# Optimization experiments

Hardware: AMD Instinct MI355X
Metric: run time of the kernel (lower is better)

The kernel has to match this reference:

```python
import jax, jax.numpy as jnp
import numpy as np

B, S, E = 2, 2048, 1024
H = 16
D = E // H  # head_dim = 64


def setup_inputs() -> dict:
    key = jax.random.key(0)
    ks = jax.random.split(key, 11)
    s = 1.0 / np.sqrt(E)
    return {
        "x": jax.random.normal(ks[0], (B, S, E), dtype=jnp.float32),
        "Wq": jax.random.uniform(ks[1], (E, E), jnp.float32, -s, s),
        "bq": jnp.zeros((E,), jnp.float32),
        "Wk": jax.random.uniform(ks[2], (E, E), jnp.float32, -s, s),
        "bk": jnp.zeros((E,), jnp.float32),
        "Wv": jax.random.uniform(ks[3], (E, E), jnp.float32, -s, s),
        "bv": jnp.zeros((E,), jnp.float32),
        "Wo": jax.random.uniform(ks[4], (E, E), jnp.float32, -s, s),
        "bo": jnp.zeros((E,), jnp.float32),
        "J_attn": jax.random.normal(ks[5], (H, D, D), jnp.float32) * 0.02,
        "lambda_attn": jnp.float32(0.5),
    }


def reference(x, Wq, bq, Wk, bk, Wv, bv, Wo, bo, J_attn, lambda_attn):
    b, s, _ = x.shape
    scale = jnp.sqrt(jnp.float32(D))

    def split_heads(y):  # [b,s,E] -> [b,H,s,D]
        return y.reshape(b, s, H, D).transpose(0, 2, 1, 3)

    Q = split_heads(x @ Wq.T + bq)
    K = split_heads(x @ Wk.T + bk)
    V = split_heads(x @ Wv.T + bv)

    attn_scores = jnp.einsum('bhid,bhjd->bhij', Q, K) / scale

    Qn = jnp.tanh(Q)
    Kn = jnp.tanh(K)
    # fold J into Qn first (small [H,D,D] contraction), then one big matmul
    QJ = jnp.einsum('bhid,hde->bhie', Qn, J_attn)
    delta = jnp.einsum('bhie,bhje->bhij', QJ, Kn)

    attn_scores = attn_scores + lambda_attn * delta
    attn_probs = jax.nn.softmax(attn_scores, axis=-1)

    out = jnp.einsum('bhij,bhjd->bhid', attn_probs, V)
    out = out.transpose(0, 2, 1, 3).reshape(b, s, E)
    return out @ Wo.T + bo
```

## Files before the change

kernel.cpp:

```cpp
#include <hip/hip_runtime.h>
#include <math.h>

#define NH 16

typedef __bf16 bf16x8 __attribute__((ext_vector_type(8)));
typedef float f32x4 __attribute__((ext_vector_type(4)));

__device__ __forceinline__ unsigned short f2bf(float f) {
  unsigned u = __float_as_uint(f);
  u += 0x7fffu + ((u >> 16) & 1u);
  return (unsigned short)(u >> 16);
}
__device__ __forceinline__ float bf2f(unsigned short h) {
  return __uint_as_float(((unsigned)h) << 16);
}
__device__ __forceinline__ float fast_tanh16(float x) {
  return 1.f - 2.f / (__expf(16.f * x) + 1.f);
}
__device__ __forceinline__ void gl_lds16(const void* g, void* l) {
  __builtin_amdgcn_global_load_lds((const __attribute__((address_space(1))) void*)g,
                                   (__attribute__((address_space(3))) void*)l, 16, 0, 0);
}
union Frag8 { bf16x8 v; unsigned short u[8]; };
union FragU { bf16x8 v; unsigned u[4]; };
union FragQ { bf16x8 v; unsigned long long q[2]; };

__global__ __launch_bounds__(256) void prep_all(const float* __restrict__ x,
                                                const float* __restrict__ Wq,
                                                const float* __restrict__ Wk,
                                                const float* __restrict__ Wv,
                                                const float* __restrict__ Wo,
                                                unsigned short* __restrict__ xh,
                                                unsigned short* __restrict__ wcat3,
                                                unsigned short* __restrict__ wocat)
{
  const int bid = blockIdx.x, tid = threadIdx.x;
  if (bid < 4096) {
    int i = bid * 256 + tid;
    float4 v = *(const float4*)&x[(size_t)i*4];
    ushort4 o;
    o.x = f2bf(v.x); o.y = f2bf(v.y); o.z = f2bf(v.z); o.w = f2bf(v.w);
    *(ushort4*)&xh[(size_t)i*4] = o;
  } else if (bid < 7168) {
    int i = (bid - 4096) * 256 + tid;
    int sel = i >> 18, loc = i & 262143;
    const float* src = (sel == 0) ? Wq : (sel == 1) ? Wk : Wv;
    float4 v = *(const float4*)&src[(size_t)loc*4];
    ushort4 o;
    o.x = f2bf(v.x); o.y = f2bf(v.y); o.z = f2bf(v.z); o.w = f2bf(v.w);
    *(ushort4*)&wcat3[(size_t)i*4] = o;
  } else {
    int i = (bid - 7168) * 256 + tid;
    int r = i >> 8, c = i & 255;
    float4 v = *(const float4*)&Wo[(size_t)r*1024 + c*4];
    ushort4 hi, lo;
    hi.x = f2bf(v.x); lo.x = f2bf(v.x - bf2f(hi.x));
    hi.y = f2bf(v.y); lo.y = f2bf(v.y - bf2f(hi.y));
    hi.z = f2bf(v.z); lo.z = f2bf(v.z - bf2f(hi.z));
    hi.w = f2bf(v.w); lo.w = f2bf(v.w - bf2f(hi.w));
    *(ushort4*)&wocat[(size_t)r*2048 + c*4]        = hi;
    *(ushort4*)&wocat[(size_t)r*2048 + 1024 + c*4] = lo;
  }
}

__global__ __launch_bounds__(256) void prep_jt(const float* __restrict__ J,
                                               const float* __restrict__ lam_p,
                                               unsigned short* __restrict__ Jt)
{
  __shared__ float T[64][65];
  const int h = blockIdx.x, tid = threadIdx.x;
  const float lam = lam_p[0];
#pragma unroll
  for (int c = 0; c < 4; ++c) {
    int i = tid + c*256;
    int d = i >> 4, e4 = i & 15;
    float4 v = *(const float4*)&J[(size_t)h*4096 + d*64 + e4*4];
    T[d][e4*4+0] = v.x; T[d][e4*4+1] = v.y; T[d][e4*4+2] = v.z; T[d][e4*4+3] = v.w;
  }
  __syncthreads();
  const int e = tid >> 2, d0 = (tid & 3) * 16;
#pragma unroll
  for (int j4 = 0; j4 < 4; ++j4) {
    ushort4 o;
    o.x = f2bf(lam * T[d0+j4*4+0][e]);
    o.y = f2bf(lam * T[d0+j4*4+1][e]);
    o.z = f2bf(lam * T[d0+j4*4+2][e]);
    o.w = f2bf(lam * T[d0+j4*4+3][e]);
    *(ushort4*)&Jt[((size_t)h*64 + e)*64 + d0 + j4*4] = o;
  }
}

__global__ __launch_bounds__(256) void gemm_qkv(const unsigned short* __restrict__ A,
                                                const unsigned short* __restrict__ W,
                                                const float* __restrict__ bq,
                                                const float* __restrict__ bk,
                                                const float* __restrict__ bv,
                                                unsigned short* __restrict__ Qcat,
                                                unsigned short* __restrict__ Kcat,
                                                unsigned short* __restrict__ Vt)
{
  __shared__ unsigned short S[16384];
  const int tid = threadIdx.x, lane = tid & 63, wq = tid >> 6;
  const int l15 = lane & 15, lq = lane >> 4;
  const int n0 = blockIdx.x * 128, m0 = blockIdx.y * 128;
  const int wr = (wq & 1) * 64, wc = (wq >> 1) * 64;
  const int mode = n0 >> 10;

  f32x4 acc[4][4];
#pragma unroll
  for (int mb = 0; mb < 4; ++mb)
#pragma unroll
    for (int nb = 0; nb < 4; ++nb) { f32x4 z = {0.f,0.f,0.f,0.f}; acc[mb][nb] = z; }

  const unsigned short* mat = (wq < 2) ? A : W;
  const int rbase = (wq < 2) ? m0 : n0;
  unsigned short* lbase = S + (wq >> 1) * 8192;
  const int srow = lane >> 3, sslot = lane & 7;

  for (int k0 = 0; k0 < 1024; k0 += 64) {
    __syncthreads();
#pragma unroll
    for (int t = 0; t < 8; ++t) {
      int row = (wq & 1) * 64 + t*8 + srow;
      int chunk = sslot ^ (row & 7);
      gl_lds16(mat + (size_t)(rbase + row)*1024 + k0 + chunk*8,
               lbase + ((wq & 1) * 64 + t*8) * 64);
    }
    __syncthreads();
#pragma unroll
    for (int kk = 0; kk < 2; ++kk) {
      int c = kk*4 + lq;
      bf16x8 af[4], bf_[4];
#pragma unroll
      for (int mb = 0; mb < 4; ++mb) {
        int m = wr + mb*16 + l15;
        af[mb] = *(const bf16x8*)&S[m*64 + (c ^ (m & 7))*8];
      }
#pragma unroll
      for (int nb = 0; nb < 4; ++nb) {
        int n = wc + nb*16 + l15;
        bf_[nb] = *(const bf16x8*)&S[8192 + n*64 + (c ^ (n & 7))*8];
      }
#pragma unroll
      for (int mb = 0; mb < 4; ++mb)
#pragma unroll
        for (int nb = 0; nb < 4; ++nb)
          acc[mb][nb] = __builtin_amdgcn_mfma_f32_16x16x32_bf16(af[mb], bf_[nb], acc[mb][nb], 0,0,0);
    }
  }

  const float* bias = (mode == 0) ? bq : (mode == 1) ? bk : bv;
  float bvv[4];
#pragma unroll
  for (int nb = 0; nb < 4; ++nb) bvv[nb] = bias[((n0 & 1023) + wc + nb*16 + l15)];

  if (mode == 2) {
#pragma unroll
    for (int mb = 0; mb < 4; ++mb) {
      int mrow = m0 + wr + mb*16 + lq*4;
      int b = mrow >> 11, s0 = mrow & 2047;
#pragma unroll
      for (int nb = 0; nb < 4; ++nb) {
        int n = (n0 & 1023) + wc + nb*16 + l15;
        int h = n >> 6, d = n & 63;
        ushort4 o;
        o.x = f2bf(acc[mb][nb][0] + bvv[nb]);
        o.y = f2bf(acc[mb][nb][1] + bvv[nb]);
        o.z = f2bf(acc[mb][nb][2] + bvv[nb]);
        o.w = f2bf(acc[mb][nb][3] + bvv[nb]);
        *(ushort4*)&Vt[((size_t)(b*NH + h)*64 + d)*2048 + s0] = o;
      }
    }
    return;
  }

#pragma unroll
  for (int mb = 0; mb < 4; ++mb) {
#pragma unroll
    for (int r = 0; r < 4; ++r) {
      int m = m0 + wr + mb*16 + lq*4 + r;
      int b = m >> 11, s = m & 2047;
#pragma unroll
      for (int nb = 0; nb < 4; ++nb) {
        float v = acc[mb][nb][r] + bvv[nb];
        int n = (n0 & 1023) + wc + nb*16 + l15;
        int h = n >> 6, d = n & 63;
        size_t row = ((size_t)(b*NH + h)*2048 + s)*128;
        if (mode == 0) {
          Qcat[row + d] = f2bf(v * 0.125f);
        } else {
          Kcat[row + d]      = f2bf(v);
          Kcat[row + 64 + d] = f2bf(1.f - 2.f / (__expf(2.f*v) + 1.f));
        }
      }
    }
  }
}

__global__ __launch_bounds__(256) void build_qj2(unsigned short* __restrict__ Qcat,
                                                 const unsigned short* __restrict__ Jt)
{
  const int tid = threadIdx.x, lane = tid & 63, wq = tid >> 6;
  const int l15 = lane & 15, lq = lane >> 4;
  const int bh = blockIdx.y, row0 = blockIdx.x * 128;
  const int h = bh & (NH-1);

  bf16x8 jf[4][2];
#pragma unroll
  for (int nb = 0; nb < 4; ++nb)
#pragma unroll
    for (int kst = 0; kst < 2; ++kst)
      jf[nb][kst] = *(const bf16x8*)&Jt[((size_t)h*64 + nb*16 + l15)*64 + kst*32 + lq*8];

  Frag8 af[2][2];
#pragma unroll
  for (int mb = 0; mb < 2; ++mb) {
    const unsigned short* qp = Qcat + ((size_t)(bh*2048 + row0 + wq*32 + mb*16 + l15))*128 + lq*8;
#pragma unroll
    for (int kst = 0; kst < 2; ++kst) {
      Frag8 raw;
      raw.v = *(const bf16x8*)(qp + kst*32);
#pragma unroll
      for (int j = 0; j < 8; ++j) {
        float t = fast_tanh16(bf2f(raw.u[j]));
        af[mb][kst].u[j] = (unsigned short)(__float_as_uint(t) >> 16);
      }
    }
  }

  f32x4 acc[2][4];
#pragma unroll
  for (int mb = 0; mb < 2; ++mb)
#pragma unroll
    for (int nb = 0; nb < 4; ++nb) { f32x4 z = {0.f,0.f,0.f,0.f}; acc[mb][nb] = z; }
#pragma unroll
  for (int kst = 0; kst < 2; ++kst)
#pragma unroll
    for (int mb = 0; mb < 2; ++mb)
#pragma unroll
      for (int nb = 0; nb < 4; ++nb)
        acc[mb][nb] = __builtin_amdgcn_mfma_f32_16x16x32_bf16(af[mb][kst].v, jf[nb][kst], acc[mb][nb], 0,0,0);

#pragma unroll
  for (int mb = 0; mb < 2; ++mb)
#pragma unroll
    for (int r = 0; r < 4; ++r) {
      size_t rowb = ((size_t)(bh*2048 + row0 + wq*32 + mb*16 + lq*4 + r))*128 + 64;
#pragma unroll
      for (int nb = 0; nb < 4; ++nb)
        Qcat[rowb + nb*16 + l15] = f2bf(acc[mb][nb][r]);
    }
}

__global__ __launch_bounds__(256, 4) void flash7(
    const unsigned short* __restrict__ Qcat, const unsigned short* __restrict__ Kcat,
    const unsigned short* __restrict__ Vt, float* __restrict__ OP0,
    float* __restrict__ OP1, float* __restrict__ OP2, float* __restrict__ lpart)
{
  __shared__ unsigned short Ks[64*128];
  __shared__ unsigned short Vs[64*64];
  const int tid = threadIdx.x, lane = tid & 63, wq = tid >> 6;
  const int l15 = lane & 15, lq = lane >> 4;
  const int bid = blockIdx.x;
  const int bh = (((bid >> 3) & 3) << 3) | (bid & 7);
  const int inner = bid >> 5;
  const int row0 = (inner & 15) * 128;
  const int ks = inner >> 4;
  const int jt0 = ks * 11;
  const int jtN = jt0 + ((ks < 2) ? 11 : 10);

  Frag8 qf[2][4];
#pragma unroll
  for (int nb = 0; nb < 2; ++nb) {
    const unsigned short* qp = Qcat + ((size_t)(bh*2048 + row0 + wq*32 + nb*16 + l15))*128 + lq*8;
#pragma unroll
    for (int kst = 0; kst < 4; ++kst)
      qf[nb][kst].v = *(const bf16x8*)(qp + kst*32);
  }

  f32x4 o[4][2];
  float lp[2] = {0.f, 0.f};
#pragma unroll
  for (int db = 0; db < 4; ++db)
#pragma unroll
    for (int nb = 0; nb < 2; ++nb) { f32x4 z = {0.f,0.f,0.f,0.f}; o[db][nb] = z; }

  const unsigned short* kgb = Kcat + ((size_t)bh*2048)*128;
  const unsigned short* vg  = Vt + (size_t)bh*64*2048;

  for (int jt = jt0; jt < jtN; ++jt) {
    __syncthreads();
#pragma unroll
    for (int t = 0; t < 4; ++t) {
      int g = (wq*4 + t)*4 + (lane >> 4);
      int slot = lane & 15;
      int chunk = (slot & 8) | ((slot ^ g) & 7);
      gl_lds16(kgb + (size_t)(jt*64 + g)*128 + chunk*8, Ks + (wq*4 + t)*512);
    }
#pragma unroll
    for (int t = 0; t < 2; ++t) {
      int rv = (wq*2 + t)*8 + (lane >> 3);
      int chunk = (lane & 7) ^ (rv & 7);
      gl_lds16(vg + (size_t)rv*2048 + jt*64 + chunk*8, Vs + (wq*2 + t)*512);
    }
    __syncthreads();

#pragma unroll
    for (int t = 0; t < 2; ++t) {
      unsigned P2[2][2][2];
#pragma unroll
      for (int kk = 0; kk < 2; ++kk) {
        const int kb = 2*t + kk;
        bf16x8 af[4];
#pragma unroll
        for (int kst = 0; kst < 4; ++kst) {
          int key = kb*16 + l15;
          int c = kst*4 + lq;
          int slot = (c & 8) | ((c ^ key) & 7);
          af[kst] = *(const bf16x8*)&Ks[key*128 + slot*8];
        }
        f32x4 s[2];
        { f32x4 z = {0.f,0.f,0.f,0.f}; s[0] = z; s[1] = z; }
#pragma unroll
        for (int kst = 0; kst < 4; ++kst) {
          s[0] = __builtin_amdgcn_mfma_f32_16x16x32_bf16(af[kst], qf[0][kst].v, s[0], 0,0,0);
          s[1] = __builtin_amdgcn_mfma_f32_16x16x32_bf16(af[kst], qf[1][kst].v, s[1], 0,0,0);
        }
#pragma unroll
        for (int nb = 0; nb < 2; ++nb) {
          float e0 = __expf(s[nb][0]), e1 = __expf(s[nb][1]);
          float e2 = __expf(s[nb][2]), e3 = __expf(s[nb][3]);
          unsigned pk0 = __builtin_amdgcn_perm(__float_as_uint(e1), __float_as_uint(e0), 0x07060302u);
          unsigned pk1 = __builtin_amdgcn_perm(__float_as_uint(e3), __float_as_uint(e2), 0x07060302u);
          lp[nb] += __uint_as_float(pk0 << 16) + __uint_as_float(pk0 & 0xffff0000u)
                  + __uint_as_float(pk1 << 16) + __uint_as_float(pk1 & 0xffff0000u);
          P2[nb][kk][0] = pk0;
          P2[nb][kk][1] = pk1;
        }
      }

      FragU bfr[2];
#pragma unroll
      for (int nb = 0; nb < 2; ++nb) {
        bfr[nb].u[0] = P2[nb][0][0];
        bfr[nb].u[1] = P2[nb][0][1];
        bfr[nb].u[2] = P2[nb][1][0];
        bfr[nb].u[3] = P2[nb][1][1];
      }
      const int c0 = 4*t + (lq >> 1);
      const int woff = 4*(lq & 1);
#pragma unroll
      for (int db = 0; db < 4; ++db) {
        int d = db*16 + l15;
        FragQ va;
        va.q[0] = *(const unsigned long long*)&Vs[d*64 + ((c0     ^ (d & 7))*8) + woff];
        va.q[1] = *(const unsigned long long*)&Vs[d*64 + (((c0+2) ^ (d & 7))*8) + woff];
        o[db][0] = __builtin_amdgcn_mfma_f32_16x16x32_bf16(va.v, bfr[0].v, o[db][0], 0,0,0);
        o[db][1] = __builtin_amdgcn_mfma_f32_16x16x32_bf16(va.v, bfr[1].v, o[db][1], 0,0,0);
      }
    }
  }

  float* OP = (ks == 0) ? OP0 : (ks == 1) ? OP1 : OP2;
#pragma unroll
  for (int nb = 0; nb < 2; ++nb) {
    float rs = lp[nb];
    rs += __shfl_xor(rs, 16, 64);
    rs += __shfl_xor(rs, 32, 64);
    int qrow = row0 + wq*32 + nb*16 + l15;
    if (lq == 0) lpart[(size_t)ks*65536 + bh*2048 + qrow] = rs;
#pragma unroll
    for (int db = 0; db < 4; ++db)
#pragma unroll
      for (int r = 0; r < 4; ++r) {
        int d = db*16 + lq*4 + r;
        OP[(size_t)(bh*64 + d)*2048 + qrow] = o[db][nb][r];
      }
  }
}

__global__ __launch_bounds__(256) void combine3(const float* __restrict__ OP0,
                                                const float* __restrict__ OP1,
                                                const float* __restrict__ OP2,
                                                const float* __restrict__ lpart,
                                                unsigned short* __restrict__ attcat)
{
  __shared__ float Ts[64*68];
  __shared__ float Ls[64];
  const int tid = threadIdx.x;
  const int bh = blockIdx.y, s0 = blockIdx.x * 64;
  const int b = bh >> 4, h = bh & (NH-1);
#pragma unroll
  for (int c = 0; c < 4; ++c) {
    int fid = tid + c*256;
    int d = fid >> 4, s4 = fid & 15;
    size_t gi = ((size_t)(bh*64 + d))*2048 + s0 + s4*4;
    float4 a = *(const float4*)&OP0[gi];
    float4 bb = *(const float4*)&OP1[gi];
    float4 cc = *(const float4*)&OP2[gi];
    Ts[(s4*4+0)*68 + d] = a.x + bb.x + cc.x;
    Ts[(s4*4+1)*68 + d] = a.y + bb.y + cc.y;
    Ts[(s4*4+2)*68 + d] = a.z + bb.z + cc.z;
    Ts[(s4*4+3)*68 + d] = a.w + bb.w + cc.w;
  }
  if (tid < 64) {
    size_t li = (size_t)bh*2048 + s0 + tid;
    Ls[tid] = lpart[li] + lpart[65536 + li] + lpart[131072 + li];
  }
  __syncthreads();
  const int sl = tid >> 2, d0 = (tid & 3) * 16;
  const float inv = 1.f / Ls[sl];
  const size_t rb = ((size_t)(b*2048 + s0 + sl))*2048 + h*64;
#pragma unroll
  for (int j4 = 0; j4 < 4; ++j4) {
    float4 t = *(const float4*)&Ts[sl*68 + d0 + j4*4];
    float v0 = t.x*inv, v1 = t.y*inv, v2 = t.z*inv, v3 = t.w*inv;
    ushort4 hi, lo;
    hi.x = f2bf(v0); lo.x = f2bf(v0 - bf2f(hi.x));
    hi.y = f2bf(v1); lo.y = f2bf(v1 - bf2f(hi.y));
    hi.z = f2bf(v2); lo.z = f2bf(v2 - bf2f(hi.z));
    hi.w = f2bf(v3); lo.w = f2bf(v3 - bf2f(hi.w));
    *(ushort4*)&attcat[rb + d0 + j4*4]        = hi;
    *(ushort4*)&attcat[rb + 1024 + d0 + j4*4] = lo;
  }
}

__global__ __launch_bounds__(256) void gemm3(const unsigned short* __restrict__ A,
                                             const unsigned short* __restrict__ W,
                                             const float* __restrict__ bias,
                                             float* __restrict__ out)
{
  __shared__ unsigned short S[16384];
  const int tid = threadIdx.x, lane = tid & 63, wq = tid >> 6;
  const int l15 = lane & 15, lq = lane >> 4;
  const int n0 = blockIdx.x * 64, m0 = blockIdx.y * 64;
  const int wr = (wq & 1) * 32, wc = (wq >> 1) * 32;

  f32x4 acc[2][2];
#pragma unroll
  for (int mb = 0; mb < 2; ++mb)
#pragma unroll
    for (int nb = 0; nb < 2; ++nb) { f32x4 z = {0.f,0.f,0.f,0.f}; acc[mb][nb] = z; }

  const unsigned short* mat = (wq < 2) ? A : W;
  const int rbase = (wq < 2) ? m0 : n0;
  const int koffadd = (wq & 1) * 1024;
  unsigned short* lbase = S + wq * 4096;
  const int srow = lane >> 3, sslot = lane & 7;

  for (int k0 = 0; k0 < 1024; k0 += 64) {
    __syncthreads();
#pragma unroll
    for (int t = 0; t < 8; ++t) {
      int row = t*8 + srow;
      int chunk = sslot ^ (row & 7);
      gl_lds16(mat + (size_t)(rbase + row)*2048 + koffadd + k0 + chunk*8, lbase + t*512);
    }
    __syncthreads();
#pragma unroll
    for (int kk = 0; kk < 2; ++kk) {
      int c = kk*4 + lq;
      bf16x8 ah[2], al[2], bh_[2], bl_[2];
#pragma unroll
      for (int mb = 0; mb < 2; ++mb) {
        int m = wr + mb*16 + l15;
        int so = (c ^ (m & 7))*8;
        ah[mb] = *(const bf16x8*)&S[m*64 + so];
        al[mb] = *(const bf16x8*)&S[4096 + m*64 + so];
      }
#pragma unroll
      for (int nb = 0; nb < 2; ++nb) {
        int n = wc + nb*16 + l15;
        int so = (c ^ (n & 7))*8;
        bh_[nb] = *(const bf16x8*)&S[8192  + n*64 + so];
        bl_[nb] = *(const bf16x8*)&S[12288 + n*64 + so];
      }
#pragma unroll
      for (int mb = 0; mb < 2; ++mb)
#pragma unroll
        for (int nb = 0; nb < 2; ++nb) {
          acc[mb][nb] = __builtin_amdgcn_mfma_f32_16x16x32_bf16(ah[mb], bh_[nb], acc[mb][nb], 0,0,0);
          acc[mb][nb] = __builtin_amdgcn_mfma_f32_16x16x32_bf16(al[mb], bh_[nb], acc[mb][nb], 0,0,0);
          acc[mb][nb] = __builtin_amdgcn_mfma_f32_16x16x32_bf16(ah[mb], bl_[nb], acc[mb][nb], 0,0,0);
        }
    }
  }

  float bvv[2];
#pragma unroll
  for (int nb = 0; nb < 2; ++nb) bvv[nb] = bias[n0 + wc + nb*16 + l15];
#pragma unroll
  for (int mb = 0; mb < 2; ++mb)
#pragma unroll
    for (int r = 0; r < 4; ++r) {
      int m = m0 + wr + mb*16 + lq*4 + r;
#pragma unroll
      for (int nb = 0; nb < 2; ++nb) {
        int n = n0 + wc + nb*16 + l15;
        out[(size_t)m*1024 + n] = acc[mb][nb][r] + bvv[nb];
      }
    }
}

extern "C" void kernel_launch(void* const* d_in, const int* in_sizes, int n_in,
                              void* d_out, int out_size, void* d_ws, size_t ws_size,
                              hipStream_t stream)
{
  const float* x   = (const float*)d_in[0];
  const float* Wq  = (const float*)d_in[1];
  const float* bq  = (const float*)d_in[2];
  const float* Wk  = (const float*)d_in[3];
  const float* bk  = (const float*)d_in[4];
  const float* Wv  = (const float*)d_in[5];
  const float* bv  = (const float*)d_in[6];
  const float* Wo  = (const float*)d_in[7];
  const float* bo  = (const float*)d_in[8];
  const float* J   = (const float*)d_in[9];
  const float* lam = (const float*)d_in[10];

  char* p = (char*)d_ws;
  char* regionA = p;
  unsigned short* xh     = (unsigned short*)p;  p += (size_t)4096*1024*2;
  unsigned short* wcat3  = (unsigned short*)p;  p += (size_t)3072*1024*2;
  unsigned short* Jt     = (unsigned short*)p;  p += (size_t)16*64*64*2;
  p += (size_t)2*1024*1024;
  unsigned short* Qcat   = (unsigned short*)p;  p += (size_t)65536*128*2;
  unsigned short* Kcat   = (unsigned short*)p;  p += (size_t)65536*128*2;
  unsigned short* Vt     = (unsigned short*)p;  p += (size_t)32*64*2048*2;
  unsigned short* wocat  = (unsigned short*)p;  p += (size_t)1024*2048*2;
  unsigned short* attcat = (unsigned short*)p;  p += (size_t)4096*2048*2;
  float*          OP0    = (float*)p;           p += (size_t)32*64*2048*4;
  float*          OP1    = (float*)p;           p += (size_t)32*64*2048*4;
  float*          lpart  = (float*)p;           p += (size_t)3*65536*4;
  float*          OP2    = (float*)regionA;
  float* out = (float*)d_out;

  dim3 blk(256);

  prep_all<<<dim3(8192), blk, 0, stream>>>(x, Wq, Wk, Wv, Wo, xh, wcat3, wocat);
  prep_jt<<<dim3(16), blk, 0, stream>>>(J, lam, Jt);
  gemm_qkv<<<dim3(24, 32), blk, 0, stream>>>(xh, wcat3, bq, bk, bv, Qcat, Kcat, Vt);
  build_qj2<<<dim3(16, 32), blk, 0, stream>>>(Qcat, Jt);
  flash7<<<dim3(1536), blk, 0, stream>>>(Qcat, Kcat, Vt, OP0, OP1, OP2, lpart);
  combine3<<<dim3(32, 32), blk, 0, stream>>>(OP0, OP1, OP2, lpart, attcat);
  gemm3<<<dim3(16, 64), blk, 0, stream>>>(attcat, wocat, bo, out);
}
```

Before: 258.1 us.

## Use exp2 softmax with folded log2e, MFMA row sums, double-buffered 128x128 output GEMM

Folds log2(e) into the Q scale and the lambda-scaled J so the flash kernel can use the native exp2 instruction, and swaps divisions for hardware reciprocals. The per-lane softmax denominator accumulation and its shuffles are replaced by an extra MFMA against a ones vector. The output projection becomes a 512-thread, 128x128-tile kernel with double-buffered LDS staging that overlaps loads with MFMA. The larger tile and 128 KB of shared memory lower occupancy and leave only 256 blocks, which may underfill the GPU.

```diff
diff --git a/kernel.cpp b/kernel.cpp
--- a/kernel.cpp
+++ b/kernel.cpp
@@ -14,8 +14,11 @@
 __device__ __forceinline__ float bf2f(unsigned short h) {
   return __uint_as_float(((unsigned)h) << 16);
 }
+__device__ __forceinline__ float fexp2(float x) {
+  return __builtin_amdgcn_exp2f(x);
+}
 __device__ __forceinline__ float fast_tanh16(float x) {
-  return 1.f - 2.f / (__expf(16.f * x) + 1.f);
+  return 1.f - 2.f * __builtin_amdgcn_rcpf(fexp2(16.f * x) + 1.f);
 }
 __device__ __forceinline__ void gl_lds16(const void* g, void* l) {
   __builtin_amdgcn_global_load_lds((const __attribute__((address_space(1))) void*)g,
@@ -69,7 +72,7 @@
 {
   __shared__ float T[64][65];
   const int h = blockIdx.x, tid = threadIdx.x;
-  const float lam = lam_p[0];
+  const float lam = lam_p[0] * 1.44269504f;
 #pragma unroll
   for (int c = 0; c < 4; ++c) {
     int i = tid + c*256;
@@ -187,10 +190,10 @@
         int h = n >> 6, d = n & 63;
         size_t row = ((size_t)(b*NH + h)*2048 + s)*128;
         if (mode == 0) {
-          Qcat[row + d] = f2bf(v * 0.125f);
+          Qcat[row + d] = f2bf(v * 0.18033688f);
         } else {
           Kcat[row + d]      = f2bf(v);
-          Kcat[row + 64 + d] = f2bf(1.f - 2.f / (__expf(2.f*v) + 1.f));
+          Kcat[row + 64 + d] = f2bf(1.f - 2.f * __builtin_amdgcn_rcpf(__expf(2.f*v) + 1.f));
         }
       }
     }
@@ -278,8 +281,13 @@
       qf[nb][kst].v = *(const bf16x8*)(qp + kst*32);
   }
 
+  FragU ones;
+  ones.u[0] = 0x3F803F80u; ones.u[1] = 0x3F803F80u;
+  ones.u[2] = 0x3F803F80u; ones.u[3] = 0x3F803F80u;
+
   f32x4 o[4][2];
-  float lp[2] = {0.f, 0.f};
+  f32x4 lacc[2];
+  { f32x4 z = {0.f,0.f,0.f,0.f}; lacc[0] = z; lacc[1] = z; }
 #pragma unroll
   for (int db = 0; db < 4; ++db)
 #pragma unroll
@@ -328,14 +336,10 @@
         }
 #pragma unroll
         for (int nb = 0; nb < 2; ++nb) {
-          float e0 = __expf(s[nb][0]), e1 = __expf(s[nb][1]);
-          float e2 = __expf(s[nb][2]), e3 = __expf(s[nb][3]);
-          unsigned pk0 = __builtin_amdgcn_perm(__float_as_uint(e1), __float_as_uint(e0), 0x07060302u);
-          unsigned pk1 = __builtin_amdgcn_perm(__float_as_uint(e3), __float_as_uint(e2), 0x07060302u);
-          lp[nb] += __uint_as_float(pk0 << 16) + __uint_as_float(pk0 & 0xffff0000u)
-                  + __uint_as_float(pk1 << 16) + __uint_as_float(pk1 & 0xffff0000u);
-          P2[nb][kk][0] = pk0;
-          P2[nb][kk][1] = pk1;
+          float e0 = fexp2(s[nb][0]), e1 = fexp2(s[nb][1]);
+          float e2 = fexp2(s[nb][2]), e3 = fexp2(s[nb][3]);
+          P2[nb][kk][0] = __builtin_amdgcn_perm(__float_as_uint(e1), __float_as_uint(e0), 0x07060302u);
+          P2[nb][kk][1] = __builtin_amdgcn_perm(__float_as_uint(e3), __float_as_uint(e2), 0x07060302u);
         }
       }
 
@@ -347,6 +351,9 @@
         bfr[nb].u[2] = P2[nb][1][0];
         bfr[nb].u[3] = P2[nb][1][1];
       }
+      lacc[0] = __builtin_amdgcn_mfma_f32_16x16x32_bf16(ones.v, bfr[0].v, lacc[0], 0,0,0);
+      lacc[1] = __builtin_amdgcn_mfma_f32_16x16x32_bf16(ones.v, bfr[1].v, lacc[1], 0,0,0);
+
       const int c0 = 4*t + (lq >> 1);
       const int woff = 4*(lq & 1);
 #pragma unroll
@@ -364,11 +371,8 @@
   float* OP = (ks == 0) ? OP0 : (ks == 1) ? OP1 : OP2;
 #pragma unroll
   for (int nb = 0; nb < 2; ++nb) {
-    float rs = lp[nb];
-    rs += __shfl_xor(rs, 16, 64);
-    rs += __shfl_xor(rs, 32, 64);
     int qrow = row0 + wq*32 + nb*16 + l15;
-    if (lq == 0) lpart[(size_t)ks*65536 + bh*2048 + qrow] = rs;
+    if (lq == 0) lpart[(size_t)ks*65536 + bh*2048 + qrow] = lacc[nb][0];
 #pragma unroll
     for (int db = 0; db < 4; ++db)
 #pragma unroll
@@ -425,58 +429,68 @@
   }
 }
 
-__global__ __launch_bounds__(256) void gemm3(const unsigned short* __restrict__ A,
-                                             const unsigned short* __restrict__ W,
-                                             const float* __restrict__ bias,
-                                             float* __restrict__ out)
-{
-  __shared__ unsigned short S[16384];
-  const int tid = threadIdx.x, lane = tid & 63, wq = tid >> 6;
+__global__ __launch_bounds__(512) void gemm3b(const unsigned short* __restrict__ A,
+                                              const unsigned short* __restrict__ W,
+                                              const float* __restrict__ bias,
+                                              float* __restrict__ out)
+{
+  __shared__ unsigned short S[65536];
+  const int tid = threadIdx.x, lane = tid & 63, wid = tid >> 6;
   const int l15 = lane & 15, lq = lane >> 4;
-  const int n0 = blockIdx.x * 64, m0 = blockIdx.y * 64;
-  const int wr = (wq & 1) * 32, wc = (wq >> 1) * 32;
-
-  f32x4 acc[2][2];
-#pragma unroll
-  for (int mb = 0; mb < 2; ++mb)
+  const int n0 = blockIdx.x * 128, m0 = blockIdx.y * 128;
+  const int wrow = wid >> 2, wcol = wid & 3;
+
+  f32x4 acc[4][2];
+#pragma unroll
+  for (int mb = 0; mb < 4; ++mb)
 #pragma unroll
     for (int nb = 0; nb < 2; ++nb) { f32x4 z = {0.f,0.f,0.f,0.f}; acc[mb][nb] = z; }
 
-  const unsigned short* mat = (wq < 2) ? A : W;
-  const int rbase = (wq < 2) ? m0 : n0;
-  const int koffadd = (wq & 1) * 1024;
-  unsigned short* lbase = S + wq * 4096;
+  const int region = wid >> 1;
+  const unsigned short* mat = (region < 2) ? A : W;
+  const int rbase = (region < 2) ? m0 : n0;
+  const int koff  = (region & 1) * 1024;
+  const int rhalf = (wid & 1) * 64;
   const int srow = lane >> 3, sslot = lane & 7;
 
+  auto STAGE = [&](int buf, int k0) {
+    unsigned short* lb = S + buf*32768 + region*8192 + rhalf*64;
+#pragma unroll
+    for (int t = 0; t < 8; ++t) {
+      int row = rhalf + t*8 + srow;
+      int chunk = sslot ^ (row & 7);
+      gl_lds16(mat + (size_t)(rbase + row)*2048 + koff + k0 + chunk*8,
+               lb + t*512);
+    }
+  };
+
+  int cur = 0;
+  STAGE(0, 0);
+  __syncthreads();
+
   for (int k0 = 0; k0 < 1024; k0 += 64) {
-    __syncthreads();
-#pragma unroll
-    for (int t = 0; t < 8; ++t) {
-      int row = t*8 + srow;
-      int chunk = sslot ^ (row & 7);
-      gl_lds16(mat + (size_t)(rbase + row)*2048 + koffadd + k0 + chunk*8, lbase + t*512);
-    }
-    __syncthreads();
+    if (k0 + 64 < 1024) STAGE(cur ^ 1, k0 + 64);
+    const unsigned short* Sc = S + cur*32768;
 #pragma unroll
     for (int kk = 0; kk < 2; ++kk) {
       int c = kk*4 + lq;
-      bf16x8 ah[2], al[2], bh_[2], bl_[2];
-#pragma unroll
-      for (int mb = 0; mb < 2; ++mb) {
-        int m = wr + mb*16 + l15;
+      bf16x8 ah[4], al[4], bh_[2], bl_[2];
+#pragma unroll
+      for (int mb = 0; mb < 4; ++mb) {
+        int m = wrow*64 + mb*16 + l15;
         int so = (c ^ (m & 7))*8;
-        ah[mb] = *(const bf16x8*)&S[m*64 + so];
-        al[mb] = *(const bf16x8*)&S[4096 + m*64 + so];
+        ah[mb] = *(const bf16x8*)&Sc[m*64 + so];
+        al[mb] = *(const bf16x8*)&Sc[8192 + m*64 + so];
       }
 #pragma unroll
       for (int nb = 0; nb < 2; ++nb) {
-        int n = wc + nb*16 + l15;
+        int n = wcol*32 + nb*16 + l15;
         int so = (c ^ (n & 7))*8;
-        bh_[nb] = *(const bf16x8*)&S[8192  + n*64 + so];
-        bl_[nb] = *(const bf16x8*)&S[12288 + n*64 + so];
-      }
-#pragma unroll
-      for (int mb = 0; mb < 2; ++mb)
+        bh_[nb] = *(const bf16x8*)&Sc[16384 + n*64 + so];
+        bl_[nb] = *(const bf16x8*)&Sc[24576 + n*64 + so];
+      }
+#pragma unroll
+      for (int mb = 0; mb < 4; ++mb)
 #pragma unroll
         for (int nb = 0; nb < 2; ++nb) {
           acc[mb][nb] = __builtin_amdgcn_mfma_f32_16x16x32_bf16(ah[mb], bh_[nb], acc[mb][nb], 0,0,0);
@@ -484,19 +498,21 @@
           acc[mb][nb] = __builtin_amdgcn_mfma_f32_16x16x32_bf16(ah[mb], bl_[nb], acc[mb][nb], 0,0,0);
         }
     }
+    __syncthreads();
+    cur ^= 1;
   }
 
   float bvv[2];
 #pragma unroll
-  for (int nb = 0; nb < 2; ++nb) bvv[nb] = bias[n0 + wc + nb*16 + l15];
-#pragma unroll
-  for (int mb = 0; mb < 2; ++mb)
+  for (int nb = 0; nb < 2; ++nb) bvv[nb] = bias[n0 + wcol*32 + nb*16 + l15];
+#pragma unroll
+  for (int mb = 0; mb < 4; ++mb)
 #pragma unroll
     for (int r = 0; r < 4; ++r) {
-      int m = m0 + wr + mb*16 + lq*4 + r;
+      int m = m0 + wrow*64 + mb*16 + lq*4 + r;
 #pragma unroll
       for (int nb = 0; nb < 2; ++nb) {
-        int n = n0 + wc + nb*16 + l15;
+        int n = n0 + wcol*32 + nb*16 + l15;
         out[(size_t)m*1024 + n] = acc[mb][nb][r] + bvv[nb];
       }
     }
@@ -543,5 +559,5 @@
   build_qj2<<<dim3(16, 32), blk, 0, stream>>>(Qcat, Jt);
   flash7<<<dim3(1536), blk, 0, stream>>>(Qcat, Kcat, Vt, OP0, OP1, OP2, lpart);
   combine3<<<dim3(32, 32), blk, 0, stream>>>(OP0, OP1, OP2, lpart, attcat);
-  gemm3<<<dim3(16, 64), blk, 0, stream>>>(attcat, wocat, bo, out);
-}
+  gemm3b<<<dim3(8, 32), dim3(512), 0, stream>>>(attcat, wocat, bo, out);
+}
```

New measurement: 247.3 us. 4.2% less time.
